# Kernel tuning notes

Measured on AMD Instinct MI355X. Metric: run time of the kernel, lower is better.

Reference implementation:

```python
import jax, jax.numpy as jnp
import numpy as np

POT_BETA = 0.5
ONS_MIN_D = 0.1
DT = 0.01
B, N, H = 65536, 32, 128  # batch, nVar (n_dim), hidden width


def f_act(x):
    r = jax.nn.relu(x)
    r2 = jax.nn.relu(x - 0.5)
    return r * r - r2 * r2


def setup_inputs() -> dict:
    key = jax.random.key(0)
    ks = jax.random.split(key, 14)

    def xav(k, shape, gain=0.1):
        fan_out, fan_in = shape
        lim = gain * np.sqrt(6.0 / (fan_in + fan_out))
        return jax.random.uniform(k, shape, jnp.float32, -lim, lim)

    def ubias(k, shape, hi=0.05):
        return jax.random.uniform(k, shape, jnp.float32, 0.0, hi)

    return {
        "z0": jax.random.normal(ks[0], (B, N), jnp.float32),
        "noise": jax.random.normal(ks[1], (B, N), jnp.float32),
        "W0": xav(ks[2], (H, N)),      # baselayer[0]
        "b0": ubias(ks[3], (H,)),
        "W1": xav(ks[4], (H, H)),      # baselayer[1] (ResNet)
        "b1": ubias(ks[5], (H,)),
        "Wm": xav(ks[6], (N * N, H)),  # MatLayer
        "bm": jax.random.normal(ks[7], (N * N,), jnp.float32) * 0.1,
        "Wp": xav(ks[8], (N, H)),      # PotLayer
        "bp": ubias(ks[9], (N,), 0.1),
        "Wpl": xav(ks[10], (N, N)),    # PotLinear
        "bpl": ubias(ks[11], (N,), 0.1),
        "sigma_kernel": jnp.ones((N,), jnp.float32),  # constant_diagonal DiffusitivityNet
    }


def reference(z0, noise, W0, b0, W1, b1, Wm, bm, Wp, bp, Wpl, bpl, sigma_kernel):
    n = z0.shape[-1]

    def hidden(x):
        h = f_act(x @ W0.T + b0)
        h = f_act(h @ W1.T + b1) + h  # ResNet skip on layer 1
        return h

    def pot_scalar(xi):  # xi: [n] -> scalar potential V for one sample
        h = hidden(xi)
        pot = h @ Wp.T + bp + xi @ Wpl.T + bpl
        return jnp.sum(pot * pot) + POT_BETA * jnp.sum(xi * xi)

    # g = -dV/dx, per sample (torch.autograd.grad of summed V == per-sample grads)
    g = -jax.vmap(jax.grad(pot_scalar))(z0)  # [B, n]

    h = hidden(z0)  # [B, H]
    matA = (h @ Wm.T + bm).reshape(-1, n, n)  # [B, n, n]
    AL = jnp.tril(matA)
    AU = jnp.triu(matA, 1)
    # MW = antisymmetric(AU) + PSD(AL @ AL^T)
    MW = (AU - jnp.swapaxes(AU, 1, 2)) + jnp.einsum('bik,bjk->bij', AL, AL)
    drift = jnp.einsum('bij,bj->bi', MW, g) + ONS_MIN_D * g  # [B, n]

    # constant_diagonal sigma: einsum('ijk,ik->ij', diag(kernel), noise) == kernel * noise
    z1 = z0 + drift * DT + (noise * sigma_kernel) * jnp.sqrt(jnp.float32(DT))
    return z1
```

## Files before the change

kernel.cpp:

```cpp
#include <hip/hip_runtime.h>
#include <stdint.h>

typedef unsigned int u32;
typedef unsigned short u16;
typedef __attribute__((ext_vector_type(8))) short bf16x8;
typedef __attribute__((ext_vector_type(4))) float f32x4;

#define N_DIM 32
#define H_DIM 128
#define SPW 4
#define SBLK 32
#define NTHR 512
#define AB_RS 34
#define AB_SS 1090

#define CW2    0
#define CW0F   16384
#define CW1F   16896
#define CW1T   18944
#define CWPF   20992
#define CWPT   21504
#define CWPLF  22016
#define CWPLT  22144
#define CW0T   22272
#define CIDT   22784
#define CEND   22912

__device__ __forceinline__ float bflo(u32 u) { return __uint_as_float(u << 16); }
__device__ __forceinline__ float bfhi(u32 u) { return __uint_as_float(u & 0xffff0000u); }
__device__ __forceinline__ float bf1(u16 u) { return __uint_as_float(((u32)u) << 16); }
__device__ __forceinline__ u16 f2bf(float f) {
    u32 u = __float_as_uint(f);
    u += 0x7fffu + ((u >> 16) & 1u);
    return (u16)(u >> 16);
}
__device__ __forceinline__ u32 cvtpk(float a, float b) {
    u32 r;
    asm("v_cvt_pk_bf16_f32 %0, %1, %2" : "=v"(r) : "v"(a), "v"(b));
    return r;
}
__device__ __forceinline__ float factf(float x) {
    float r = fmaxf(x, 0.f), r2 = fmaxf(x - 0.5f, 0.f);
    return r * r - r2 * r2;
}
__device__ __forceinline__ float dact(float x) {
    return 2.f * fminf(fmaxf(x, 0.f), 0.5f);
}

template<bool BF> __device__ __forceinline__ float ld1(const void* p, int i) {
    if constexpr (BF) return __uint_as_float(((u32)(((const u16*)p)[i])) << 16);
    else              return ((const float*)p)[i];
}
template<bool BF> __device__ __forceinline__ float2 ld2(const void* p, int i) {
    if constexpr (BF) { u32 u = *(const u32*)((const u16*)p + i); return make_float2(bflo(u), bfhi(u)); }
    else              { return *(const float2*)((const float*)p + i); }
}
template<bool BF> __device__ __forceinline__ float4 ld4(const void* p, int i) {
    if constexpr (BF) { uint2 u = *(const uint2*)((const u16*)p + i);
        return make_float4(bflo(u.x), bfhi(u.x), bflo(u.y), bfhi(u.y)); }
    else              { return *(const float4*)((const float*)p + i); }
}
template<bool BF> __device__ __forceinline__ void st2(void* p, int i, float a, float b) {
    if constexpr (BF) { u32 o = (u32)f2bf(a) | ((u32)f2bf(b) << 16); *(u32*)((u16*)p + i) = o; }
    else              { *(float2*)((float*)p + i) = make_float2(a, b); }
}

__global__ __launch_bounds__(256) void repack_all(
    const void* W0, const void* W1, const void* Wm,
    const void* Wp, const void* Wpl, const void* sig, u16* W)
{
    const int c = blockIdx.x * 256 + threadIdx.x;
    if (c >= CEND) return;
    const bool bf = (*(const u32*)sig) != 0x3F800000u;
    u16 o[8];
    if (c >= CIDT) {
        const int local = c - CIDT, ln = local & 63, nt = local >> 6;
        const int k = (ln >> 4) * 8, n = nt * 16 + (ln & 15);
#pragma unroll
        for (int e = 0; e < 8; ++e) o[e] = (k + e == n) ? (u16)0x3F80 : (u16)0;
    } else {
        const void* src; int LD, local, KS; bool T;
        if      (c < CW0F)  { src = Wm;  LD = 128; T = false; local = c - CW2;   KS = 4; }
        else if (c < CW1F)  { src = W0;  LD = 32;  T = false; local = c - CW0F;  KS = 1; }
        else if (c < CW1T)  { src = W1;  LD = 128; T = false; local = c - CW1F;  KS = 4; }
        else if (c < CWPF)  { src = W1;  LD = 128; T = true;  local = c - CW1T;  KS = 4; }
        else if (c < CWPT)  { src = Wp;  LD = 128; T = false; local = c - CWPF;  KS = 4; }
        else if (c < CWPLF) { src = Wp;  LD = 128; T = true;  local = c - CWPT;  KS = 1; }
        else if (c < CWPLT) { src = Wpl; LD = 32;  T = false; local = c - CWPLF; KS = 1; }
        else if (c < CW0T)  { src = Wpl; LD = 32;  T = true;  local = c - CWPLT; KS = 1; }
        else                { src = W0;  LD = 32;  T = true;  local = c - CW0T;  KS = 4; }
        const int ln = local & 63;
        const int ks = (local >> 6) & (KS - 1);
        const int nt = local / (KS * 64);
        const int k  = ks * 32 + (ln >> 4) * 8;
        const int n  = nt * 16 + (ln & 15);
#pragma unroll
        for (int e = 0; e < 8; ++e) {
            const int kk = k + e;
            const int si = T ? (kk * LD + n) : (n * LD + kk);
            o[e] = bf ? ((const u16*)src)[si] : f2bf(((const float*)src)[si]);
        }
    }
    u32* dst = (u32*)(W + (size_t)c * 8);
    dst[0] = (u32)o[0] | ((u32)o[1] << 16);
    dst[1] = (u32)o[2] | ((u32)o[3] << 16);
    dst[2] = (u32)o[4] | ((u32)o[5] << 16);
    dst[3] = (u32)o[6] | ((u32)o[7] << 16);
}

#define MFMA16(a, b, c) __builtin_amdgcn_mfma_f32_16x16x32_bf16((a), (b), (c), 0, 0, 0)

template<bool BF>
__device__ __forceinline__ void body(
    const void* z0, const void* noise, const void* b0, const void* b1,
    const void* bm, const void* bp, const void* bpl, const void* sig,
    const bf16x8* WS, void* out, int Btot,
    u16* Ab2, u16* h2b, u16* g2)
{
    const int t = threadIdx.x;
    const int w = t >> 6, l = t & 63;
    const int cn = l & 15, lh = l >> 4;
    const int pidx = blockIdx.x * NTHR + t;
    const int npair = Btot * (N_DIM / 2);

    u16* h2a = Ab2;
    u16* gaf = Ab2 + 4096;
    u16* x2  = Ab2 + 8192;
    u16* u2  = Ab2 + 9216;

    const float2 xz = (pidx < npair) ? ld2<BF>(z0, 2 * pidx) : make_float2(0.f, 0.f);
    {
        const int s = t >> 4, j0 = 2 * (t & 15);
        *(u32*)&x2[((j0 >> 3) * 32 + s) * 8 + (j0 & 7)] =
            (u32)f2bf(xz.x) | ((u32)f2bf(xz.y) << 16);
    }
    __syncthreads();

    const bf16x8 afx0 = *(const bf16x8*)&x2[(lh * 32 + cn) * 8];
    const bf16x8 afx1 = *(const bf16x8*)&x2[(lh * 32 + 16 + cn) * 8];

    float h0r[2][4], d0r[2][4], d1r[2][4], ghr[2][4];

    {
        const bf16x8 wb = WS[CW0F + w * 64 + l];
        const float b0v = ld1<BF>(b0, w * 16 + cn);
        const int n = w * 16 + cn;
#pragma unroll
        for (int st = 0; st < 2; ++st) {
            f32x4 acc = {0.f, 0.f, 0.f, 0.f};
            acc = MFMA16(st ? afx1 : afx0, wb, acc);
#pragma unroll
            for (int r = 0; r < 4; ++r) {
                const float a0 = acc[r] + b0v;
                h0r[st][r] = factf(a0); d0r[st][r] = dact(a0);
                const int s = st * 16 + lh * 4 + r;
                h2a[((n >> 3) * 32 + s) * 8 + (n & 7)] = f2bf(h0r[st][r]);
            }
        }
    }
    __syncthreads();

    {
        const float b1v = ld1<BF>(b1, w * 16 + cn);
        const int n = w * 16 + cn;
        bf16x8 wb[4];
#pragma unroll
        for (int ks = 0; ks < 4; ++ks) wb[ks] = WS[CW1F + (w * 4 + ks) * 64 + l];
#pragma unroll
        for (int st = 0; st < 2; ++st) {
            f32x4 acc = {0.f, 0.f, 0.f, 0.f};
#pragma unroll
            for (int ks = 0; ks < 4; ++ks) {
                const bf16x8 af = *(const bf16x8*)&h2a[((ks * 4 + lh) * 32 + st * 16 + cn) * 8];
                acc = MFMA16(af, wb[ks], acc);
            }
#pragma unroll
            for (int r = 0; r < 4; ++r) {
                const float a1 = acc[r] + b1v;
                d1r[st][r] = dact(a1);
                const int s = st * 16 + lh * 4 + r;
                h2b[((n >> 3) * 32 + s) * 8 + (n & 7)] = f2bf(factf(a1) + h0r[st][r]);
            }
        }
    }
    __syncthreads();

    if (w < 4) {
        const int st = w >> 1, ntP = w & 1;
        const int n = ntP * 16 + cn;
        f32x4 acc = {0.f, 0.f, 0.f, 0.f};
#pragma unroll
        for (int ks = 0; ks < 4; ++ks) {
            const bf16x8 af = *(const bf16x8*)&h2b[((ks * 4 + lh) * 32 + st * 16 + cn) * 8];
            acc = MFMA16(af, WS[CWPF + (ntP * 4 + ks) * 64 + l], acc);
        }
        acc = MFMA16(st ? afx1 : afx0, WS[CWPLF + ntP * 64 + l], acc);
        const float pb = ld1<BF>(bp, n) + ld1<BF>(bpl, n);
#pragma unroll
        for (int r = 0; r < 4; ++r) {
            const int s = st * 16 + lh * 4 + r;
            u2[((n >> 3) * 32 + s) * 8 + (n & 7)] = f2bf(2.f * (acc[r] + pb));
        }
    }
    __syncthreads();

    const bf16x8 afu0 = *(const bf16x8*)&u2[(lh * 32 + cn) * 8];
    const bf16x8 afu1 = *(const bf16x8*)&u2[(lh * 32 + 16 + cn) * 8];

    {
        const bf16x8 wb = WS[CWPT + w * 64 + l];
        const int n = w * 16 + cn;
#pragma unroll
        for (int st = 0; st < 2; ++st) {
            f32x4 acc = {0.f, 0.f, 0.f, 0.f};
            acc = MFMA16(st ? afu1 : afu0, wb, acc);
#pragma unroll
            for (int r = 0; r < 4; ++r) {
                ghr[st][r] = acc[r];
                const int s = st * 16 + lh * 4 + r;
                h2a[((n >> 3) * 32 + s) * 8 + (n & 7)] = f2bf(acc[r] * d1r[st][r]);
            }
        }
    }
    __syncthreads();

    {
        const int n = w * 16 + cn;
        bf16x8 wb[4];
#pragma unroll
        for (int ks = 0; ks < 4; ++ks) wb[ks] = WS[CW1T + (w * 4 + ks) * 64 + l];
#pragma unroll
        for (int st = 0; st < 2; ++st) {
            f32x4 acc = {0.f, 0.f, 0.f, 0.f};
#pragma unroll
            for (int ks = 0; ks < 4; ++ks) {
                const bf16x8 af = *(const bf16x8*)&h2a[((ks * 4 + lh) * 32 + st * 16 + cn) * 8];
                acc = MFMA16(af, wb[ks], acc);
            }
#pragma unroll
            for (int r = 0; r < 4; ++r) {
                const float ga0v = (acc[r] + ghr[st][r]) * d0r[st][r];
                const int s = st * 16 + lh * 4 + r;
                gaf[((n >> 3) * 32 + s) * 8 + (n & 7)] = f2bf(ga0v);
            }
        }
    }
    __syncthreads();

    if (w < 4) {
        const int st = w >> 1, ntP = w & 1;
        const int n = ntP * 16 + cn;
        f32x4 acc = {0.f, 0.f, 0.f, 0.f};
#pragma unroll
        for (int ks = 0; ks < 4; ++ks) {
            const bf16x8 af = *(const bf16x8*)&gaf[((ks * 4 + lh) * 32 + st * 16 + cn) * 8];
            acc = MFMA16(af, WS[CW0T + (ntP * 4 + ks) * 64 + l], acc);
        }
        acc = MFMA16(st ? afu1 : afu0, WS[CWPLT + ntP * 64 + l], acc);
        acc = MFMA16(st ? afx1 : afx0, WS[CIDT + ntP * 64 + l], acc);
#pragma unroll
        for (int r = 0; r < 4; ++r) {
            const int s = st * 16 + lh * 4 + r;
            g2[s * N_DIM + n] = f2bf(-acc[r]);
        }
    }
    __syncthreads();

    {
        bf16x8 bh0[4], bh1[4];
#pragma unroll
        for (int ks = 0; ks < 4; ++ks) {
            bh0[ks] = *(const bf16x8*)&h2b[((ks * 4 + lh) * 32 + cn) * 8];
            bh1[ks] = *(const bf16x8*)&h2b[((ks * 4 + lh) * 32 + 16 + cn) * 8];
        }
#pragma unroll 2
        for (int mt = 0; mt < 8; ++mt) {
            const int mtg = w * 8 + mt;
            bf16x8 wa[4];
#pragma unroll
            for (int ks = 0; ks < 4; ++ks) wa[ks] = WS[CW2 + (mtg * 4 + ks) * 64 + l];
            const int m0 = mtg * 16 + lh * 4;
            const float4 bmv = ld4<BF>(bm, m0);
            const int i  = mtg >> 1;
            const int jb = (mtg & 1) * 16 + lh * 4;
#pragma unroll
            for (int st = 0; st < 2; ++st) {
                f32x4 acc = {0.f, 0.f, 0.f, 0.f};
                acc = MFMA16(wa[0], st ? bh1[0] : bh0[0], acc);
                acc = MFMA16(wa[1], st ? bh1[1] : bh0[1], acc);
                acc = MFMA16(wa[2], st ? bh1[2] : bh0[2], acc);
                acc = MFMA16(wa[3], st ? bh1[3] : bh0[3], acc);
                const int s = st * 16 + cn;
                u32* dst = (u32*)&Ab2[s * AB_SS + i * AB_RS + jb];
                dst[0] = cvtpk(acc[0] + bmv.x, acc[1] + bmv.y);
                dst[1] = cvtpk(acc[2] + bmv.z, acc[3] + bmv.w);
            }
        }
    }
    __syncthreads();

    float* ubuf = (float*)h2b;
    float* dbuf = ubuf + SBLK * N_DIM;
    {
        const int c = l & 31, ih = l >> 5;
#pragma unroll
        for (int ss = 0; ss < SPW; ++ss) {
            const int s = w * SPW + ss;
            const u16* As = &Ab2[s * AB_SS];
            const u16* gs = &g2[s * N_DIM];
            float yp = 0.f, tp = 0.f;
#pragma unroll
            for (int r = 0; r < 16; ++r) {
                const int i = ih * 16 + r;
                const float a = bf1(As[i * AB_RS + c]);
                const float gi = bf1(gs[i]);
                if (i >= c) yp = fmaf(a, gi, yp); else tp = fmaf(a, gi, tp);
            }
            const float yv = yp + __shfl_xor(yp, 32);
            const float tv = tp + __shfl_xor(tp, 32);
            if (l < 32) { ubuf[s * N_DIM + c] = yv; dbuf[s * N_DIM + c] = -tv; }
            float au = 0.f;
#pragma unroll
            for (int q = 0; q < 8; ++q) {
                const int j0 = ih * 16 + 2 * q;
                const u32 av = *(const u32*)&As[c * AB_RS + j0];
                const u32 gv = *(const u32*)&gs[j0];
                const float2 yv2 = *(const float2*)&ubuf[s * N_DIM + j0];
                const float s0 = (j0     > c) ? bflo(gv) : yv2.x;
                const float s1 = (j0 + 1 > c) ? bfhi(gv) : yv2.y;
                au = fmaf(bflo(av), s0, au);
                au = fmaf(bfhi(av), s1, au);
            }
            au += __shfl_xor(au, 32);
            if (l < 32) dbuf[s * N_DIM + c] += au;
        }
    }

    if (pidx < npair) {
        const float2 nz2 = ld2<BF>(noise, 2 * pidx);
        const int e0 = 2 * t;
        const int jj = e0 & 31;
        const float sg0 = ld1<BF>(sig, jj), sg1 = ld1<BF>(sig, jj + 1);
        const u32 gv = *(const u32*)&g2[e0];
        const float dr0 = dbuf[e0]     + 0.1f * bflo(gv);
        const float dr1 = dbuf[e0 + 1] + 0.1f * bfhi(gv);
        const float z10 = xz.x + dr0 * 0.01f + nz2.x * sg0 * 0.1f;
        const float z11 = xz.y + dr1 * 0.01f + nz2.y * sg1 * 0.1f;
        st2<BF>(out, 2 * pidx, z10, z11);
    }
}

__global__ __launch_bounds__(512, 4) void onsager_step(
    const void* z0, const void* noise, const void* b0, const void* b1,
    const void* bm, const void* bp, const void* bpl, const void* sig,
    const void* ws, void* out, int Btot)
{
    __shared__ __align__(16) u16 Ab2[SBLK * AB_SS];
    __shared__ __align__(16) u16 h2b[SBLK * H_DIM];
    __shared__ __align__(16) u16 g2 [SBLK * N_DIM];

    const u32 sigbits = *(const u32*)sig;
    if (sigbits == 0x3F800000u)
        body<false>(z0, noise, b0, b1, bm, bp, bpl, sig, (const bf16x8*)ws, out, Btot,
                    Ab2, h2b, g2);
    else
        body<true >(z0, noise, b0, b1, bm, bp, bpl, sig, (const bf16x8*)ws, out, Btot,
                    Ab2, h2b, g2);
}

extern "C" void kernel_launch(void* const* d_in, const int* in_sizes, int n_in,
                              void* d_out, int out_size, void* d_ws, size_t ws_size,
                              hipStream_t stream) {
    const void* z0  = d_in[0];
    const void* nz  = d_in[1];
    const void* W0  = d_in[2];
    const void* b0  = d_in[3];
    const void* W1  = d_in[4];
    const void* b1  = d_in[5];
    const void* Wm  = d_in[6];
    const void* bm  = d_in[7];
    const void* Wp  = d_in[8];
    const void* bp  = d_in[9];
    const void* Wpl = d_in[10];
    const void* bpl = d_in[11];
    const void* sig = d_in[12];

    const int Btot = in_sizes[0] / N_DIM;
    u16* W = (u16*)d_ws;

    repack_all<<<dim3((CEND + 255) / 256), dim3(256), 0, stream>>>(W0, W1, Wm, Wp, Wpl, sig, W);

    dim3 grid((Btot + SBLK - 1) / SBLK), block(NTHR);
    onsager_step<<<grid, block, 0, stream>>>(z0, nz, b0, b1, bm, bp, bpl, sig,
                                             d_ws, d_out, Btot);
}
```

Before: 147.7 us.

## Swizzle per-sample A matrix in LDS and use MFMA identity transpose for column pass

The per-sample 32x32 A matrix is now stored in LDS with a dense row stride and an XOR-like phase swizzle of 8-element chunks, replacing the padded stride. The column-wise pass (tril(A)^T g) uses MFMA against an identity matrix to obtain transposed fragments rather than strided scalar LDS reads. The row pass reads 16-byte vectors. The repack kernel is also split across 4x more threads, each writing one 32-bit word. The intent is fewer LDS bank conflicts and fewer scalar LDS loads, at the cost of extra MFMAs and shuffles.

```diff
diff --git a/kernel.cpp b/kernel.cpp
--- a/kernel.cpp
+++ b/kernel.cpp
@@ -11,8 +11,7 @@
 #define SPW 4
 #define SBLK 32
 #define NTHR 512
-#define AB_RS 34
-#define AB_SS 1090
+#define A_SS 1032
 
 #define CW2    0
 #define CW0F   16384
@@ -69,15 +68,16 @@
     const void* W0, const void* W1, const void* Wm,
     const void* Wp, const void* Wpl, const void* sig, u16* W)
 {
-    const int c = blockIdx.x * 256 + threadIdx.x;
-    if (c >= CEND) return;
+    const int tid = blockIdx.x * 256 + threadIdx.x;
+    if (tid >= CEND * 4) return;
+    const int c = tid >> 2, pe = tid & 3;
     const bool bf = (*(const u32*)sig) != 0x3F800000u;
-    u16 o[8];
+    u16 o0, o1;
     if (c >= CIDT) {
         const int local = c - CIDT, ln = local & 63, nt = local >> 6;
-        const int k = (ln >> 4) * 8, n = nt * 16 + (ln & 15);
-#pragma unroll
-        for (int e = 0; e < 8; ++e) o[e] = (k + e == n) ? (u16)0x3F80 : (u16)0;
+        const int k = (ln >> 4) * 8 + pe * 2, n = nt * 16 + (ln & 15);
+        o0 = (k == n)     ? (u16)0x3F80 : (u16)0;
+        o1 = (k + 1 == n) ? (u16)0x3F80 : (u16)0;
     } else {
         const void* src; int LD, local, KS; bool T;
         if      (c < CW0F)  { src = Wm;  LD = 128; T = false; local = c - CW2;   KS = 4; }
@@ -92,20 +92,14 @@
         const int ln = local & 63;
         const int ks = (local >> 6) & (KS - 1);
         const int nt = local / (KS * 64);
-        const int k  = ks * 32 + (ln >> 4) * 8;
+        const int k  = ks * 32 + (ln >> 4) * 8 + pe * 2;
         const int n  = nt * 16 + (ln & 15);
-#pragma unroll
-        for (int e = 0; e < 8; ++e) {
-            const int kk = k + e;
-            const int si = T ? (kk * LD + n) : (n * LD + kk);
-            o[e] = bf ? ((const u16*)src)[si] : f2bf(((const float*)src)[si]);
-        }
-    }
-    u32* dst = (u32*)(W + (size_t)c * 8);
-    dst[0] = (u32)o[0] | ((u32)o[1] << 16);
-    dst[1] = (u32)o[2] | ((u32)o[3] << 16);
-    dst[2] = (u32)o[4] | ((u32)o[5] << 16);
-    dst[3] = (u32)o[6] | ((u32)o[7] << 16);
+        const int s0 = T ? (k * LD + n) : (n * LD + k);
+        const int s1 = T ? ((k + 1) * LD + n) : (n * LD + k + 1);
+        if (bf) { o0 = ((const u16*)src)[s0]; o1 = ((const u16*)src)[s1]; }
+        else    { o0 = f2bf(((const float*)src)[s0]); o1 = f2bf(((const float*)src)[s1]); }
+    }
+    ((u32*)W)[(size_t)c * 4 + pe] = (u32)o0 | ((u32)o1 << 16);
 }
 
 #define MFMA16(a, b, c) __builtin_amdgcn_mfma_f32_16x16x32_bf16((a), (b), (c), 0, 0, 0)
@@ -115,7 +109,7 @@
     const void* z0, const void* noise, const void* b0, const void* b1,
     const void* bm, const void* bp, const void* bpl, const void* sig,
     const bf16x8* WS, void* out, int Btot,
-    u16* Ab2, u16* h2b, u16* g2)
+    u16* Asub, u16* h2b, u16* g2)
 {
     const int t = threadIdx.x;
     const int w = t >> 6, l = t & 63;
@@ -123,10 +117,10 @@
     const int pidx = blockIdx.x * NTHR + t;
     const int npair = Btot * (N_DIM / 2);
 
-    u16* h2a = Ab2;
-    u16* gaf = Ab2 + 4096;
-    u16* x2  = Ab2 + 8192;
-    u16* u2  = Ab2 + 9216;
+    u16* h2a = Asub;
+    u16* gaf = Asub + 4096;
+    u16* x2  = Asub + 8192;
+    u16* u2  = Asub + 8704;
 
     const float2 xz = (pidx < npair) ? ld2<BF>(z0, 2 * pidx) : make_float2(0.f, 0.f);
     {
@@ -281,8 +275,10 @@
             for (int ks = 0; ks < 4; ++ks) wa[ks] = WS[CW2 + (mtg * 4 + ks) * 64 + l];
             const int m0 = mtg * 16 + lh * 4;
             const float4 bmv = ld4<BF>(bm, m0);
-            const int i  = mtg >> 1;
-            const int jb = (mtg & 1) * 16 + lh * 4;
+            const int i   = mtg >> 1;
+            const int jb  = (mtg & 1) * 16 + lh * 4;
+            const int phys = (((jb >> 3) + (i >> 2)) & 3);
+            const int off  = jb & 7;
 #pragma unroll
             for (int st = 0; st < 2; ++st) {
                 f32x4 acc = {0.f, 0.f, 0.f, 0.f};
@@ -291,9 +287,10 @@
                 acc = MFMA16(wa[2], st ? bh1[2] : bh0[2], acc);
                 acc = MFMA16(wa[3], st ? bh1[3] : bh0[3], acc);
                 const int s = st * 16 + cn;
-                u32* dst = (u32*)&Ab2[s * AB_SS + i * AB_RS + jb];
-                dst[0] = cvtpk(acc[0] + bmv.x, acc[1] + bmv.y);
-                dst[1] = cvtpk(acc[2] + bmv.z, acc[3] + bmv.w);
+                uint2 pk;
+                pk.x = cvtpk(acc[0] + bmv.x, acc[1] + bmv.y);
+                pk.y = cvtpk(acc[2] + bmv.z, acc[3] + bmv.w);
+                *(uint2*)&Asub[s * A_SS + i * 32 + phys * 8 + off] = pk;
             }
         }
     }
@@ -302,37 +299,72 @@
     float* ubuf = (float*)h2b;
     float* dbuf = ubuf + SBLK * N_DIM;
     {
-        const int c = l & 31, ih = l >> 5;
+        const int c32 = l & 31, ih = l >> 5;
+        const bf16x8 id0 = WS[CIDT + 0 * 64 + l];
+        const bf16x8 id1 = WS[CIDT + 1 * 64 + l];
 #pragma unroll
         for (int ss = 0; ss < SPW; ++ss) {
             const int s = w * SPW + ss;
-            const u16* As = &Ab2[s * AB_SS];
-            const u16* gs = &g2[s * N_DIM];
-            float yp = 0.f, tp = 0.f;
-#pragma unroll
-            for (int r = 0; r < 16; ++r) {
-                const int i = ih * 16 + r;
-                const float a = bf1(As[i * AB_RS + c]);
-                const float gi = bf1(gs[i]);
-                if (i >= c) yp = fmaf(a, gi, yp); else tp = fmaf(a, gi, tp);
-            }
-            const float yv = yp + __shfl_xor(yp, 32);
-            const float tv = tp + __shfl_xor(tp, 32);
-            if (l < 32) { ubuf[s * N_DIM + c] = yv; dbuf[s * N_DIM + c] = -tv; }
+            const u16* As = &g2[0];
+            (void)As;
+            const u16* Ab = &Asub[s * A_SS];
+            const int ph1 = (lh + (cn >> 2)) & 3;
+            const bf16x8 af0 = *(const bf16x8*)&Ab[(cn)      * 32 + ph1 * 8];
+            const bf16x8 af1 = *(const bf16x8*)&Ab[(16 + cn) * 32 + ph1 * 8];
+            f32x4 P00 = {0.f,0.f,0.f,0.f}, P01 = {0.f,0.f,0.f,0.f};
+            f32x4 P10 = {0.f,0.f,0.f,0.f}, P11 = {0.f,0.f,0.f,0.f};
+            P00 = MFMA16(af0, id0, P00);
+            P01 = MFMA16(af0, id1, P01);
+            P10 = MFMA16(af1, id0, P10);
+            P11 = MFMA16(af1, id1, P11);
+            const u32 ga0v = *(const u32*)&g2[s * N_DIM + lh * 4];
+            const u32 ga1v = *(const u32*)&g2[s * N_DIM + lh * 4 + 2];
+            const u32 gb0v = *(const u32*)&g2[s * N_DIM + 16 + lh * 4];
+            const u32 gb1v = *(const u32*)&g2[s * N_DIM + 16 + lh * 4 + 2];
+            const float gi0[4] = {bflo(ga0v), bfhi(ga0v), bflo(ga1v), bfhi(ga1v)};
+            const float gi1[4] = {bflo(gb0v), bfhi(gb0v), bflo(gb1v), bfhi(gb1v)};
+            float yp0 = 0.f, tp0 = 0.f, yp1 = 0.f, tp1 = 0.f;
+#pragma unroll
+            for (int r = 0; r < 4; ++r) {
+                const bool ge = (lh * 4 + r >= cn);
+                yp0 = fmaf(P00[r], ge ? gi0[r] : 0.f, yp0);
+                tp0 = fmaf(P00[r], ge ? 0.f : gi0[r], tp0);
+            }
+#pragma unroll
+            for (int r = 0; r < 4; ++r) tp1 = fmaf(P01[r], gi0[r], tp1);
+#pragma unroll
+            for (int r = 0; r < 4; ++r) yp0 = fmaf(P10[r], gi1[r], yp0);
+#pragma unroll
+            for (int r = 0; r < 4; ++r) {
+                const bool ge = (lh * 4 + r >= cn);
+                yp1 = fmaf(P11[r], ge ? gi1[r] : 0.f, yp1);
+                tp1 = fmaf(P11[r], ge ? 0.f : gi1[r], tp1);
+            }
+            yp0 += __shfl_xor(yp0, 16); yp0 += __shfl_xor(yp0, 32);
+            tp0 += __shfl_xor(tp0, 16); tp0 += __shfl_xor(tp0, 32);
+            yp1 += __shfl_xor(yp1, 16); yp1 += __shfl_xor(yp1, 32);
+            tp1 += __shfl_xor(tp1, 16); tp1 += __shfl_xor(tp1, 32);
+            if (lh == 0) { ubuf[s * N_DIM + cn] = yp0;      dbuf[s * N_DIM + cn] = -tp0; }
+            if (lh == 1) { ubuf[s * N_DIM + 16 + cn] = yp1; dbuf[s * N_DIM + 16 + cn] = -tp1; }
+            const int pha = ((ih * 2 + 0) + (c32 >> 2)) & 3;
+            const int phb = ((ih * 2 + 1) + (c32 >> 2)) & 3;
+            const uint4 ra = *(const uint4*)&Ab[c32 * 32 + pha * 8];
+            const uint4 rb = *(const uint4*)&Ab[c32 * 32 + phb * 8];
+            const u32 arr[8] = {ra.x, ra.y, ra.z, ra.w, rb.x, rb.y, rb.z, rb.w};
             float au = 0.f;
 #pragma unroll
             for (int q = 0; q < 8; ++q) {
                 const int j0 = ih * 16 + 2 * q;
-                const u32 av = *(const u32*)&As[c * AB_RS + j0];
-                const u32 gv = *(const u32*)&gs[j0];
+                const u32 av = arr[q];
+                const u32 gv = *(const u32*)&g2[s * N_DIM + j0];
                 const float2 yv2 = *(const float2*)&ubuf[s * N_DIM + j0];
-                const float s0 = (j0     > c) ? bflo(gv) : yv2.x;
-                const float s1 = (j0 + 1 > c) ? bfhi(gv) : yv2.y;
+                const float s0 = (j0     > c32) ? bflo(gv) : yv2.x;
+                const float s1 = (j0 + 1 > c32) ? bfhi(gv) : yv2.y;
                 au = fmaf(bflo(av), s0, au);
                 au = fmaf(bfhi(av), s1, au);
             }
             au += __shfl_xor(au, 32);
-            if (l < 32) dbuf[s * N_DIM + c] += au;
+            if (l < 32) dbuf[s * N_DIM + c32] += au;
         }
     }
 
@@ -355,17 +387,17 @@
     const void* bm, const void* bp, const void* bpl, const void* sig,
     const void* ws, void* out, int Btot)
 {
-    __shared__ __align__(16) u16 Ab2[SBLK * AB_SS];
+    __shared__ __align__(16) u16 Asub[SBLK * A_SS];
     __shared__ __align__(16) u16 h2b[SBLK * H_DIM];
     __shared__ __align__(16) u16 g2 [SBLK * N_DIM];
 
     const u32 sigbits = *(const u32*)sig;
     if (sigbits == 0x3F800000u)
         body<false>(z0, noise, b0, b1, bm, bp, bpl, sig, (const bf16x8*)ws, out, Btot,
-                    Ab2, h2b, g2);
+                    Asub, h2b, g2);
     else
         body<true >(z0, noise, b0, b1, bm, bp, bpl, sig, (const bf16x8*)ws, out, Btot,
-                    Ab2, h2b, g2);
+                    Asub, h2b, g2);
 }
 
 extern "C" void kernel_launch(void* const* d_in, const int* in_sizes, int n_in,
@@ -388,7 +420,8 @@
     const int Btot = in_sizes[0] / N_DIM;
     u16* W = (u16*)d_ws;
 
-    repack_all<<<dim3((CEND + 255) / 256), dim3(256), 0, stream>>>(W0, W1, Wm, Wp, Wpl, sig, W);
+    repack_all<<<dim3((CEND * 4 + 255) / 256), dim3(256), 0, stream>>>(
+        W0, W1, Wm, Wp, Wpl, sig, W);
 
     dim3 grid((Btot + SBLK - 1) / SBLK), block(NTHR);
     onsager_step<<<grid, block, 0, stream>>>(z0, nz, b0, b1, bm, bp, bpl, sig,
```

Result: no change. 145.9 us (-1.2%).
